# Kernel tuning notes

Measured on AMD Instinct MI355X. Metric: run time of the kernel, lower is better.

Reference implementation:

```python
import jax, jax.numpy as jnp
import numpy as np

N_SLOTS = 256
CHANNELS = 2048

def setup_inputs() -> dict:
    key = jax.random.key(0)
    k1, k2, k3, k4 = jax.random.split(key, 4)
    B, C, H, W = 32, CHANNELS, 32, 32
    x = jax.random.normal(k1, (B, C, H, W), dtype=jnp.float32)
    slot_assign = jax.random.randint(k2, (B, H, W), 0, N_SLOTS, dtype=jnp.int32)
    # slot noise tables: alpha ~ N(1, sigma1), beta ~ N(0, sigma2)
    sigma1, sigma2 = 0.1, 0.1
    alpha = 1.0 + sigma1 * jax.random.normal(k3, (N_SLOTS, CHANNELS), dtype=jnp.float32)
    beta = sigma2 * jax.random.normal(k4, (N_SLOTS, CHANNELS), dtype=jnp.float32)
    return {"x": x, "slot_assign": slot_assign, "alpha": alpha, "beta": beta}

def reference(x, slot_assign, alpha, beta):
    # Gather per-pixel (alpha, beta) rows: [B,H,W,C] -> move C to axis 1
    a = jnp.transpose(alpha[slot_assign], (0, 3, 1, 2))  # [B,C,H,W]
    b = jnp.transpose(beta[slot_assign], (0, 3, 1, 2))   # [B,C,H,W]
    return a * x + b
```

## Files before the change

### kernel.cpp

```cpp
#include <hip/hip_runtime.h>


typedef float  f4 __attribute__((ext_vector_type(4)));
typedef int    i4 __attribute__((ext_vector_type(4)));

#define CH   2048
#define HW   1024
#define NS   256
#define CG   (CH / 4)

__global__ __launch_bounds__(256) void fa_kernel(
    const float* __restrict__ x,
    const int*   __restrict__ slot,
    const float* __restrict__ alpha,
    const float* __restrict__ beta,
    float*       __restrict__ out)
{
    __shared__ f4 lds_a[NS];
    __shared__ f4 lds_b[NS];

    const int cg = blockIdx.x & (CG - 1);
    const int b  = blockIdx.x >> 9;
    const int c0 = cg << 2;
    const int t  = threadIdx.x;
    const int p  = t << 2;

    const i4 s = *(const i4*)(slot + b * HW + p);

    const size_t base = ((size_t)b * CH + c0) * HW + p;
    f4 xv0 = __builtin_nontemporal_load((const f4*)(x + base + 0 * HW));
    f4 xv1 = __builtin_nontemporal_load((const f4*)(x + base + 1 * HW));
    f4 xv2 = __builtin_nontemporal_load((const f4*)(x + base + 2 * HW));
    f4 xv3 = __builtin_nontemporal_load((const f4*)(x + base + 3 * HW));

    lds_a[t] = *(const f4*)(alpha + (size_t)t * CH + c0);
    lds_b[t] = *(const f4*)(beta  + (size_t)t * CH + c0);

    __syncthreads();

    const f4 a0 = lds_a[s.x], a1 = lds_a[s.y], a2 = lds_a[s.z], a3 = lds_a[s.w];
    const f4 b0 = lds_b[s.x], b1 = lds_b[s.y], b2 = lds_b[s.z], b3 = lds_b[s.w];

    f4 o;
    o[0] = a0[0]*xv0[0] + b0[0]; o[1] = a1[0]*xv0[1] + b1[0];
    o[2] = a2[0]*xv0[2] + b2[0]; o[3] = a3[0]*xv0[3] + b3[0];
    __builtin_nontemporal_store(o, (f4*)(out + base + 0 * HW));

    o[0] = a0[1]*xv1[0] + b0[1]; o[1] = a1[1]*xv1[1] + b1[1];
    o[2] = a2[1]*xv1[2] + b2[1]; o[3] = a3[1]*xv1[3] + b3[1];
    __builtin_nontemporal_store(o, (f4*)(out + base + 1 * HW));

    o[0] = a0[2]*xv2[0] + b0[2]; o[1] = a1[2]*xv2[1] + b1[2];
    o[2] = a2[2]*xv2[2] + b2[2]; o[3] = a3[2]*xv2[3] + b3[2];
    __builtin_nontemporal_store(o, (f4*)(out + base + 2 * HW));

    o[0] = a0[3]*xv3[0] + b0[3]; o[1] = a1[3]*xv3[1] + b1[3];
    o[2] = a2[3]*xv3[2] + b2[3]; o[3] = a3[3]*xv3[3] + b3[3];
    __builtin_nontemporal_store(o, (f4*)(out + base + 3 * HW));
}

extern "C" void kernel_launch(void* const* d_in, const int* in_sizes, int n_in,
                              void* d_out, int out_size, void* d_ws, size_t ws_size,
                              hipStream_t stream) {
    const float* x     = (const float*)d_in[0];
    const int*   slot  = (const int*)d_in[1];
    const float* alpha = (const float*)d_in[2];
    const float* beta  = (const float*)d_in[3];
    float*       out   = (float*)d_out;

    const int B = in_sizes[0] / (CH * HW);
    dim3 grid(B * CG);
    dim3 block(256);
    fa_kernel<<<grid, block, 0, stream>>>(x, slot, alpha, beta, out);
}
```

Measured before the change: 485.5 us.

## Process eight channels per block with transposed scalar LDS tables

Each block now handles 8 channels instead of 4, which halves the grid and doubles the per-thread x loads in flight. The alpha/beta rows are stored in LDS as per-channel scalar arrays ([CPB][NS]) rather than f4 rows, and gathered with scalar LDS reads per channel. This amortizes the slot index load and the barrier over more work and changes the LDS access pattern. The cost is higher register pressure (8 f4 x values) under launch_bounds(256,4), and more LDS read instructions.

```diff
diff --git a/kernel.cpp b/kernel.cpp
--- a/kernel.cpp
+++ b/kernel.cpp
@@ -7,56 +7,61 @@
 #define CH   2048
 #define HW   1024
 #define NS   256
-#define CG   (CH / 4)
+#define CPB  8
+#define NCG  (CH / CPB)
 
-__global__ __launch_bounds__(256) void fa_kernel(
+__global__ __launch_bounds__(256, 4) void fa_kernel(
     const float* __restrict__ x,
     const int*   __restrict__ slot,
     const float* __restrict__ alpha,
     const float* __restrict__ beta,
     float*       __restrict__ out)
 {
-    __shared__ f4 lds_a[NS];
-    __shared__ f4 lds_b[NS];
+    __shared__ float lds_a[CPB][NS];
+    __shared__ float lds_b[CPB][NS];
 
-    const int cg = blockIdx.x & (CG - 1);
-    const int b  = blockIdx.x >> 9;
-    const int c0 = cg << 2;
+    const int cg = blockIdx.x & (NCG - 1);
+    const int b  = blockIdx.x >> 8;
+    const int c0 = cg * CPB;
     const int t  = threadIdx.x;
     const int p  = t << 2;
 
     const i4 s = *(const i4*)(slot + b * HW + p);
 
+    const f4 ar0 = *(const f4*)(alpha + (size_t)t * CH + c0);
+    const f4 ar1 = *(const f4*)(alpha + (size_t)t * CH + c0 + 4);
+    const f4 br0 = *(const f4*)(beta  + (size_t)t * CH + c0);
+    const f4 br1 = *(const f4*)(beta  + (size_t)t * CH + c0 + 4);
+
     const size_t base = ((size_t)b * CH + c0) * HW + p;
-    f4 xv0 = __builtin_nontemporal_load((const f4*)(x + base + 0 * HW));
-    f4 xv1 = __builtin_nontemporal_load((const f4*)(x + base + 1 * HW));
-    f4 xv2 = __builtin_nontemporal_load((const f4*)(x + base + 2 * HW));
-    f4 xv3 = __builtin_nontemporal_load((const f4*)(x + base + 3 * HW));
+    f4 xv[CPB];
+#pragma unroll
+    for (int k = 0; k < CPB; ++k)
+        xv[k] = __builtin_nontemporal_load((const f4*)(x + base + (size_t)k * HW));
 
-    lds_a[t] = *(const f4*)(alpha + (size_t)t * CH + c0);
-    lds_b[t] = *(const f4*)(beta  + (size_t)t * CH + c0);
+#pragma unroll
+    for (int k = 0; k < 4; ++k) {
+        lds_a[k][t]     = ar0[k];
+        lds_a[4 + k][t] = ar1[k];
+        lds_b[k][t]     = br0[k];
+        lds_b[4 + k][t] = br1[k];
+    }
 
     __syncthreads();
 
-    const f4 a0 = lds_a[s.x], a1 = lds_a[s.y], a2 = lds_a[s.z], a3 = lds_a[s.w];
-    const f4 b0 = lds_b[s.x], b1 = lds_b[s.y], b2 = lds_b[s.z], b3 = lds_b[s.w];
-
-    f4 o;
-    o[0] = a0[0]*xv0[0] + b0[0]; o[1] = a1[0]*xv0[1] + b1[0];
-    o[2] = a2[0]*xv0[2] + b2[0]; o[3] = a3[0]*xv0[3] + b3[0];
-    __builtin_nontemporal_store(o, (f4*)(out + base + 0 * HW));
-
-    o[0] = a0[1]*xv1[0] + b0[1]; o[1] = a1[1]*xv1[1] + b1[1];
-    o[2] = a2[1]*xv1[2] + b2[1]; o[3] = a3[1]*xv1[3] + b3[1];
-    __builtin_nontemporal_store(o, (f4*)(out + base + 1 * HW));
-
-    o[0] = a0[2]*xv2[0] + b0[2]; o[1] = a1[2]*xv2[1] + b1[2];
-    o[2] = a2[2]*xv2[2] + b2[2]; o[3] = a3[2]*xv2[3] + b3[2];
-    __builtin_nontemporal_store(o, (f4*)(out + base + 2 * HW));
-
-    o[0] = a0[3]*xv3[0] + b0[3]; o[1] = a1[3]*xv3[1] + b1[3];
-    o[2] = a2[3]*xv3[2] + b2[3]; o[3] = a3[3]*xv3[3] + b3[3];
-    __builtin_nontemporal_store(o, (f4*)(out + base + 3 * HW));
+#pragma unroll
+    for (int k = 0; k < CPB; ++k) {
+        const float a0 = lds_a[k][s.x], a1 = lds_a[k][s.y],
+                    a2 = lds_a[k][s.z], a3 = lds_a[k][s.w];
+        const float b0 = lds_b[k][s.x], b1 = lds_b[k][s.y],
+                    b2 = lds_b[k][s.z], b3 = lds_b[k][s.w];
+        f4 o;
+        o[0] = a0 * xv[k][0] + b0;
+        o[1] = a1 * xv[k][1] + b1;
+        o[2] = a2 * xv[k][2] + b2;
+        o[3] = a3 * xv[k][3] + b3;
+        __builtin_nontemporal_store(o, (f4*)(out + base + (size_t)k * HW));
+    }
 }
 
 extern "C" void kernel_launch(void* const* d_in, const int* in_sizes, int n_in,
@@ -69,7 +74,7 @@
     float*       out   = (float*)d_out;
 
     const int B = in_sizes[0] / (CH * HW);
-    dim3 grid(B * CG);
+    dim3 grid(B * NCG);
     dim3 block(256);
     fa_kernel<<<grid, block, 0, stream>>>(x, slot, alpha, beta, out);
 }
```

Result: faster. 447.7 us (-7.8%).
